# Performance work log

Hardware: AMD Instinct MI355X
Metric: run time of the kernel (lower is better)

Reference implementation:

```python
import jax, jax.numpy as jnp
import numpy as np

D_MODEL = 1024
NUM_HEADS = 16
HEAD_DIM = D_MODEL // NUM_HEADS
B, S = 4, 2048


def setup_inputs() -> dict:
    key = jax.random.key(0)
    ks = jax.random.split(key, 11)
    scale = 1.0 / np.sqrt(D_MODEL)
    inp = {
        "Q": jax.random.normal(ks[0], (B, S, D_MODEL), jnp.float32),
        "K": jax.random.normal(ks[1], (B, S, D_MODEL), jnp.float32),
        "V": jax.random.normal(ks[2], (B, S, D_MODEL), jnp.float32),
        # torch nn.Linear params: weight [out, in], bias [out]
        "WQ_w": jax.random.uniform(ks[3], (D_MODEL, D_MODEL), jnp.float32, -scale, scale),
        "WQ_b": jax.random.uniform(ks[4], (D_MODEL,), jnp.float32, -scale, scale),
        "WK_w": jax.random.uniform(ks[5], (D_MODEL, D_MODEL), jnp.float32, -scale, scale),
        "WK_b": jax.random.uniform(ks[6], (D_MODEL,), jnp.float32, -scale, scale),
        "WV_w": jax.random.uniform(ks[7], (D_MODEL, D_MODEL), jnp.float32, -scale, scale),
        "WV_b": jax.random.uniform(ks[8], (D_MODEL,), jnp.float32, -scale, scale),
        "WO_w": jax.random.uniform(ks[9], (D_MODEL, D_MODEL), jnp.float32, -scale, scale),
        "WO_b": jax.random.uniform(ks[10], (D_MODEL,), jnp.float32, -scale, scale),
    }
    return inp


def _linear(x, w, b):
    # torch Linear: y = x @ w.T + b
    return jnp.einsum("bsd,ed->bse", x, w) + b


def _split_heads(x):
    b, s, _ = x.shape
    return x.reshape(b, s, NUM_HEADS, HEAD_DIM).transpose(0, 2, 1, 3)  # [B,H,S,hd]


def reference(Q, K, V, WQ_w, WQ_b, WK_w, WK_b, WV_w, WV_b, WO_w, WO_b):
    q = _split_heads(_linear(Q, WQ_w, WQ_b))  # [B,H,S,hd]
    k = _split_heads(_linear(K, WK_w, WK_b))
    v = _split_heads(_linear(V, WV_w, WV_b))
    scale = 1.0 / jnp.sqrt(jnp.asarray(HEAD_DIM, jnp.float32))
    scores = jnp.einsum("bhqd,bhkd->bhqk", q, k) * scale  # [B,H,S,S]
    attn = jax.nn.softmax(scores, axis=-1)
    ctx = jnp.einsum("bhqk,bhkd->bhqd", attn, v)  # [B,H,S,hd]
    ctx = ctx.transpose(0, 2, 1, 3).reshape(Q.shape[0], Q.shape[1], D_MODEL)
    out = _linear(ctx, WO_w, WO_b)
    return out, attn
```

## Files before the change

kernel.cpp:

```cpp
#include <hip/hip_runtime.h>
#include <hip/hip_fp16.h>

typedef _Float16 half_t;
typedef __attribute__((ext_vector_type(8))) _Float16 half8;
typedef __attribute__((ext_vector_type(4))) _Float16 half4;
typedef __attribute__((ext_vector_type(4))) float f32x4;

#define D_MODEL 1024
#define NHEAD 16
#define HDIM 64
#define BATCH 4
#define SEQ 2048
#define M_TOTAL (BATCH*SEQ)

#define BM 128
#define BN 128
#define BKK 32
#define LDT 40

template<int OUTMODE, bool A_HALF>
__global__ __launch_bounds__(256)
void gemm_bt(const void* __restrict__ Ap, const float* __restrict__ Bp,
             const float* __restrict__ bias, void* __restrict__ outp)
{
    __shared__ half_t As[BM * LDT];
    __shared__ half_t Bs[BN * LDT];

    const int lin = blockIdx.x;
    const int swz = (lin & 7) * 64 + (lin >> 3);
    const int bm  = (swz >> 3) * BM;
    const int bn  = (swz & 7) * BN;

    const int tid  = threadIdx.x;
    const int lane = tid & 63;
    const int w    = tid >> 6;
    const int wm   = w >> 1, wn = w & 1;
    const int g    = lane >> 4, c = lane & 15;
    const int K    = 1024;

    f32x4 acc[4][4] = {};

    float4 fa[4];
    float4 fb[4];
    uint4  ha[2];

    auto load_tile = [&](int kt) {
        const int kb = kt * BKK;
        if (A_HALF) {
            const half_t* A = (const half_t*)Ap;
#pragma unroll
            for (int i = 0; i < 2; ++i) {
                const int row = (tid >> 2) + i * 64;
                const int col = (tid & 3) * 8;
                ha[i] = *(const uint4*)&A[(size_t)(bm + row) * K + kb + col];
            }
        } else {
            const float* A = (const float*)Ap;
#pragma unroll
            for (int i = 0; i < 4; ++i) {
                const int row = (tid >> 3) + i * 32;
                const int col = (tid & 7) * 4;
                fa[i] = *(const float4*)&A[(size_t)(bm + row) * K + kb + col];
            }
        }
#pragma unroll
        for (int i = 0; i < 4; ++i) {
            const int row = (tid >> 3) + i * 32;
            const int col = (tid & 7) * 4;
            fb[i] = *(const float4*)&Bp[(size_t)(bn + row) * K + kb + col];
        }
    };

    auto store_tile = [&]() {
        if (A_HALF) {
#pragma unroll
            for (int i = 0; i < 2; ++i) {
                const int row = (tid >> 2) + i * 64;
                const int col = (tid & 3) * 8;
                *(uint4*)&As[row * LDT + col] = ha[i];
            }
        } else {
#pragma unroll
            for (int i = 0; i < 4; ++i) {
                const int row = (tid >> 3) + i * 32;
                const int col = (tid & 7) * 4;
                half4 h = { (half_t)fa[i].x, (half_t)fa[i].y, (half_t)fa[i].z, (half_t)fa[i].w };
                *(half4*)&As[row * LDT + col] = h;
            }
        }
#pragma unroll
        for (int i = 0; i < 4; ++i) {
            const int row = (tid >> 3) + i * 32;
            const int col = (tid & 7) * 4;
            half4 h = { (half_t)fb[i].x, (half_t)fb[i].y, (half_t)fb[i].z, (half_t)fb[i].w };
            *(half4*)&Bs[row * LDT + col] = h;
        }
    };

    load_tile(0);
    const int NT = K / BKK;
    for (int kt = 0; kt < NT; ++kt) {
        __syncthreads();
        store_tile();
        __syncthreads();
        if (kt + 1 < NT) load_tile(kt + 1);

        half8 af[4], bf[4];
#pragma unroll
        for (int mt = 0; mt < 4; ++mt)
            af[mt] = *(const half8*)&As[(wm * 64 + mt * 16 + c) * LDT + g * 8];
#pragma unroll
        for (int nt = 0; nt < 4; ++nt)
            bf[nt] = *(const half8*)&Bs[(wn * 64 + nt * 16 + c) * LDT + g * 8];
        __builtin_amdgcn_s_setprio(1);
#pragma unroll
        for (int mt = 0; mt < 4; ++mt)
#pragma unroll
            for (int nt = 0; nt < 4; ++nt)
                acc[mt][nt] = __builtin_amdgcn_mfma_f32_16x16x32_f16(af[mt], bf[nt], acc[mt][nt], 0, 0, 0);
        __builtin_amdgcn_s_setprio(0);
    }

#pragma unroll
    for (int mt = 0; mt < 4; ++mt)
#pragma unroll
        for (int nt = 0; nt < 4; ++nt)
#pragma unroll
            for (int j = 0; j < 4; ++j) {
                const int gm = bm + wm * 64 + mt * 16 + g * 4 + j;
                const int gn = bn + wn * 64 + nt * 16 + c;
                const float val = acc[mt][nt][j] + bias[gn];
                if (OUTMODE == 0) {
                    const int b = gm >> 11, s = gm & 2047, h = gn >> 6, d = gn & 63;
                    ((half_t*)outp)[((size_t)(b * NHEAD + h) * SEQ + s) * HDIM + d] = (half_t)val;
                } else if (OUTMODE == 1) {
                    const int b = gm >> 11, s = gm & 2047, h = gn >> 6, d = gn & 63;
                    ((half_t*)outp)[((size_t)(b * NHEAD + h) * HDIM + d) * SEQ + s] = (half_t)val;
                } else {
                    ((float*)outp)[(size_t)gm * 1024 + gn] = val;
                }
            }
}

__global__ __launch_bounds__(256)
void attn_stats(const half_t* __restrict__ qh, const half_t* __restrict__ kh,
                float* __restrict__ inv_l)
{
    const int bid0 = blockIdx.x;
    const int bid  = (bid0 & 7) * 64 + (bid0 >> 3);
    const int bh   = bid >> 3;
    const int qb   = bid & 7;
    const int tid  = threadIdx.x;
    const int w    = tid >> 6;
    const int lane = tid & 63;
    const int g    = lane >> 4, c = lane & 15;
    const int wbase = qb * 256 + w * 64;
    const size_t hoff = (size_t)bh * SEQ * HDIM;

    half8 a0[4], a1[4];
#pragma unroll
    for (int rt = 0; rt < 4; ++rt) {
        a0[rt] = *(const half8*)&qh[hoff + (size_t)(wbase + rt * 16 + c) * HDIM + g * 8];
        a1[rt] = *(const half8*)&qh[hoff + (size_t)(wbase + rt * 16 + c) * HDIM + g * 8 + 32];
    }

    float l[4][4] = {};
#pragma unroll 2
    for (int t = 0; t < 128; ++t) {
        const int kc = t * 16;
        const half8 b0 = *(const half8*)&kh[hoff + (size_t)(kc + c) * HDIM + g * 8];
        const half8 b1 = *(const half8*)&kh[hoff + (size_t)(kc + c) * HDIM + g * 8 + 32];
#pragma unroll
        for (int rt = 0; rt < 4; ++rt) {
            f32x4 acc = {};
            acc = __builtin_amdgcn_mfma_f32_16x16x32_f16(a0[rt], b0, acc, 0, 0, 0);
            acc = __builtin_amdgcn_mfma_f32_16x16x32_f16(a1[rt], b1, acc, 0, 0, 0);
#pragma unroll
            for (int j = 0; j < 4; ++j)
                l[rt][j] += __expf(acc[j] * 0.125f);
        }
    }

#pragma unroll
    for (int rt = 0; rt < 4; ++rt)
#pragma unroll
        for (int j = 0; j < 4; ++j) {
            float v = l[rt][j];
            v += __shfl_xor(v, 1);
            v += __shfl_xor(v, 2);
            v += __shfl_xor(v, 4);
            v += __shfl_xor(v, 8);
            l[rt][j] = v;
        }
    if (c == 0) {
#pragma unroll
        for (int rt = 0; rt < 4; ++rt)
#pragma unroll
            for (int j = 0; j < 4; ++j)
                inv_l[bh * SEQ + wbase + rt * 16 + g * 4 + j] = 1.0f / l[rt][j];
    }
}

#define KPAD 88
#define VPAD 40
#define PPADX 40

__global__ __launch_bounds__(256)
void attn_pv(const half_t* __restrict__ qh, const half_t* __restrict__ kh,
             const half_t* __restrict__ vT, const float* __restrict__ inv_l,
             float* __restrict__ attn, half_t* __restrict__ ctx)
{
    __shared__ half_t Ks[2][32][KPAD];
    __shared__ half_t Vs[2][64][VPAD];
    __shared__ half_t pbuf[4][2][16][PPADX];

    const int bid0 = blockIdx.x;
    const int bid  = (bid0 & 7) * 128 + (bid0 >> 3);
    const int bh   = bid >> 4;
    const int qb   = bid & 15;
    const int tid  = threadIdx.x;
    const int w    = tid >> 6;
    const int lane = tid & 63;
    const int g    = lane >> 4, c = lane & 15;
    const int qbase = qb * 128;
    const int wbase = qbase + w * 32;
    const size_t hoff = (size_t)bh * SEQ * HDIM;

    half8 a0[2], a1[2];
#pragma unroll
    for (int rt = 0; rt < 2; ++rt) {
        a0[rt] = *(const half8*)&qh[hoff + (size_t)(wbase + rt * 16 + c) * HDIM + g * 8];
        a1[rt] = *(const half8*)&qh[hoff + (size_t)(wbase + rt * 16 + c) * HDIM + g * 8 + 32];
    }
    float inv[2][4];
#pragma unroll
    for (int rt = 0; rt < 2; ++rt)
#pragma unroll
        for (int j = 0; j < 4; ++j)
            inv[rt][j] = inv_l[bh * SEQ + wbase + rt * 16 + g * 4 + j];

    const half_t* vbase = vT + (size_t)bh * HDIM * SEQ;
    float* arow = attn + ((size_t)bh * SEQ + qbase) * SEQ;

    const int krow = tid >> 3;
    const int kcol = (tid & 7) * 8;
    const int vrow = tid >> 2;
    const int vcol = (tid & 3) * 8;

    const int srow = lane >> 3;
    const int scol = (lane & 7) * 4;

    uint4 kreg = *(const uint4*)&kh[hoff + (size_t)krow * HDIM + kcol];
    uint4 vreg = *(const uint4*)&vbase[(size_t)vrow * SEQ + vcol];
    *(uint4*)&Ks[0][krow][kcol] = kreg;
    *(uint4*)&Vs[0][vrow][vcol] = vreg;
    __syncthreads();

    f32x4 cacc[2][4] = {};

    for (int ch = 0; ch < 64; ++ch) {
        const int buf = ch & 1;
        const int cbase = ch * 32;

        const int ncb = (cbase + 32) & (SEQ - 1);
        kreg = *(const uint4*)&kh[hoff + (size_t)(ncb + krow) * HDIM + kcol];
        vreg = *(const uint4*)&vbase[(size_t)vrow * SEQ + ncb + vcol];

#pragma unroll
        for (int rt = 0; rt < 2; ++rt)
#pragma unroll
            for (int ct = 0; ct < 2; ++ct) {
                const half8 b0 = *(const half8*)&Ks[buf][ct * 16 + c][g * 8];
                const half8 b1 = *(const half8*)&Ks[buf][ct * 16 + c][g * 8 + 32];
                f32x4 acc = {};
                acc = __builtin_amdgcn_mfma_f32_16x16x32_f16(a0[rt], b0, acc, 0, 0, 0);
                acc = __builtin_amdgcn_mfma_f32_16x16x32_f16(a1[rt], b1, acc, 0, 0, 0);
#pragma unroll
                for (int j = 0; j < 4; ++j) {
                    const float p = __expf(acc[j] * 0.125f) * inv[rt][j];
                    pbuf[w][rt][g * 4 + j][ct * 16 + c] = (half_t)p;
                }
            }

#pragma unroll
        for (int rt = 0; rt < 2; ++rt)
#pragma unroll
            for (int hh = 0; hh < 2; ++hh) {
                const int r = hh * 8 + srow;
                const half4 hv = *(const half4*)&pbuf[w][rt][r][scol];
                f32x4 fv = { (float)hv[0], (float)hv[1], (float)hv[2], (float)hv[3] };
                *(f32x4*)&arow[(size_t)(w * 32 + rt * 16 + r) * SEQ + cbase + scol] = fv;
            }

        {
            half8 vb[4];
#pragma unroll
            for (int nt = 0; nt < 4; ++nt)
                vb[nt] = *(const half8*)&Vs[buf][nt * 16 + c][g * 8];
#pragma unroll
            for (int rt = 0; rt < 2; ++rt) {
                const half8 pa = *(const half8*)&pbuf[w][rt][c][g * 8];
                __builtin_amdgcn_s_setprio(1);
#pragma unroll
                for (int nt = 0; nt < 4; ++nt)
                    cacc[rt][nt] = __builtin_amdgcn_mfma_f32_16x16x32_f16(pa, vb[nt], cacc[rt][nt], 0, 0, 0);
                __builtin_amdgcn_s_setprio(0);
            }
        }

        __syncthreads();
        *(uint4*)&Ks[buf ^ 1][krow][kcol] = kreg;
        *(uint4*)&Vs[buf ^ 1][vrow][vcol] = vreg;
        __syncthreads();
    }

    const int b = bh >> 4, h = bh & 15;
#pragma unroll
    for (int rt = 0; rt < 2; ++rt)
#pragma unroll
        for (int nt = 0; nt < 4; ++nt)
#pragma unroll
            for (int j = 0; j < 4; ++j)
                ctx[(size_t)(b * SEQ + qbase + w * 32 + rt * 16 + g * 4 + j) * D_MODEL
                    + h * HDIM + nt * 16 + c] = (half_t)cacc[rt][nt][j];
}

extern "C" void kernel_launch(void* const* d_in, const int* in_sizes, int n_in,
                              void* d_out, int out_size, void* d_ws, size_t ws_size,
                              hipStream_t stream) {
    const float* Qin = (const float*)d_in[0];
    const float* Kin = (const float*)d_in[1];
    const float* Vin = (const float*)d_in[2];
    const float* WQw = (const float*)d_in[3];
    const float* WQb = (const float*)d_in[4];
    const float* WKw = (const float*)d_in[5];
    const float* WKb = (const float*)d_in[6];
    const float* WVw = (const float*)d_in[7];
    const float* WVb = (const float*)d_in[8];
    const float* WOw = (const float*)d_in[9];
    const float* WOb = (const float*)d_in[10];

    char* ws = (char*)d_ws;
    const size_t MB = 1024 * 1024;
    half_t* qh  = (half_t*)(ws);
    half_t* kh  = (half_t*)(ws + 16 * MB);
    half_t* vT  = (half_t*)(ws + 32 * MB);
    half_t* ctx = (half_t*)(ws + 48 * MB);

    float* out   = (float*)d_out;
    float* attn  = out + (size_t)M_TOTAL * D_MODEL;
    float* inv_l = out;

    dim3 blk(256);
    hipLaunchKernelGGL((gemm_bt<0, false>), dim3(512), blk, 0, stream, Qin, WQw, WQb, qh);
    hipLaunchKernelGGL((gemm_bt<0, false>), dim3(512), blk, 0, stream, Kin, WKw, WKb, kh);
    hipLaunchKernelGGL((gemm_bt<1, false>), dim3(512), blk, 0, stream, Vin, WVw, WVb, vT);
    hipLaunchKernelGGL(attn_stats, dim3(512), blk, 0, stream, qh, kh, inv_l);
    hipLaunchKernelGGL(attn_pv, dim3(1024), blk, 0, stream, qh, kh, vT, inv_l, attn, ctx);
    hipLaunchKernelGGL((gemm_bt<2, true>), dim3(512), blk, 0, stream, ctx, WOw, WOb, out);
}
```

Before: 513.9 us.

## Batch attn probability writes over 128-column spans and single-buffer K/V tiles

The attention-PV kernel now buffers probabilities for four 32-key chunks in a wider per-wave LDS buffer and writes the fp32 attn matrix once per 128 columns, in place of once per 32-column chunk. K/V shared tiles drop from double to single buffering, which keeps LDS usage in check despite the larger probability buffer. The goal is to separate the large attn global stores from the MFMA/exp inner loop and make them longer per row. Single buffering still relies on two barriers per chunk, and the stores now arrive in bursts.

Measured after the change: 544.8 us. +6.0%, slower.

```diff
diff --git a/kernel.cpp b/kernel.cpp
--- a/kernel.cpp
+++ b/kernel.cpp
@@ -203,16 +203,16 @@
 
 #define KPAD 88
 #define VPAD 40
-#define PPADX 40
+#define PBW  136
 
 __global__ __launch_bounds__(256)
 void attn_pv(const half_t* __restrict__ qh, const half_t* __restrict__ kh,
              const half_t* __restrict__ vT, const float* __restrict__ inv_l,
              float* __restrict__ attn, half_t* __restrict__ ctx)
 {
-    __shared__ half_t Ks[2][32][KPAD];
-    __shared__ half_t Vs[2][64][VPAD];
-    __shared__ half_t pbuf[4][2][16][PPADX];
+    __shared__ half_t Ks[32][KPAD];
+    __shared__ half_t Vs[64][VPAD];
+    __shared__ half_t pbuf[4][2][16][PBW];
 
     const int bid0 = blockIdx.x;
     const int bid  = (bid0 & 7) * 128 + (bid0 >> 3);
@@ -252,66 +252,74 @@
 
     uint4 kreg = *(const uint4*)&kh[hoff + (size_t)krow * HDIM + kcol];
     uint4 vreg = *(const uint4*)&vbase[(size_t)vrow * SEQ + vcol];
-    *(uint4*)&Ks[0][krow][kcol] = kreg;
-    *(uint4*)&Vs[0][vrow][vcol] = vreg;
+    *(uint4*)&Ks[krow][kcol] = kreg;
+    *(uint4*)&Vs[vrow][vcol] = vreg;
     __syncthreads();
 
     f32x4 cacc[2][4] = {};
 
-    for (int ch = 0; ch < 64; ++ch) {
-        const int buf = ch & 1;
-        const int cbase = ch * 32;
-
-        const int ncb = (cbase + 32) & (SEQ - 1);
-        kreg = *(const uint4*)&kh[hoff + (size_t)(ncb + krow) * HDIM + kcol];
-        vreg = *(const uint4*)&vbase[(size_t)vrow * SEQ + ncb + vcol];
-
-#pragma unroll
-        for (int rt = 0; rt < 2; ++rt)
-#pragma unroll
-            for (int ct = 0; ct < 2; ++ct) {
-                const half8 b0 = *(const half8*)&Ks[buf][ct * 16 + c][g * 8];
-                const half8 b1 = *(const half8*)&Ks[buf][ct * 16 + c][g * 8 + 32];
-                f32x4 acc = {};
-                acc = __builtin_amdgcn_mfma_f32_16x16x32_f16(a0[rt], b0, acc, 0, 0, 0);
-                acc = __builtin_amdgcn_mfma_f32_16x16x32_f16(a1[rt], b1, acc, 0, 0, 0);
-#pragma unroll
-                for (int j = 0; j < 4; ++j) {
-                    const float p = __expf(acc[j] * 0.125f) * inv[rt][j];
-                    pbuf[w][rt][g * 4 + j][ct * 16 + c] = (half_t)p;
+#pragma unroll 1
+    for (int sc = 0; sc < 16; ++sc) {
+#pragma unroll
+        for (int sub = 0; sub < 4; ++sub) {
+            const int cbase = sc * 128 + sub * 32;
+            const int ncb = (cbase + 32) & (SEQ - 1);
+
+            kreg = *(const uint4*)&kh[hoff + (size_t)(ncb + krow) * HDIM + kcol];
+            vreg = *(const uint4*)&vbase[(size_t)vrow * SEQ + ncb + vcol];
+
+#pragma unroll
+            for (int rt = 0; rt < 2; ++rt)
+#pragma unroll
+                for (int ct = 0; ct < 2; ++ct) {
+                    const half8 b0 = *(const half8*)&Ks[ct * 16 + c][g * 8];
+                    const half8 b1 = *(const half8*)&Ks[ct * 16 + c][g * 8 + 32];
+                    f32x4 acc = {};
+                    acc = __builtin_amdgcn_mfma_f32_16x16x32_f16(a0[rt], b0, acc, 0, 0, 0);
+                    acc = __builtin_amdgcn_mfma_f32_16x16x32_f16(a1[rt], b1, acc, 0, 0, 0);
+#pragma unroll
+                    for (int j = 0; j < 4; ++j) {
+                        const float p = __expf(acc[j] * 0.125f) * inv[rt][j];
+                        pbuf[w][rt][g * 4 + j][sub * 32 + ct * 16 + c] = (half_t)p;
+                    }
                 }
-            }
-
+
+            {
+                half8 vb[4];
+#pragma unroll
+                for (int nt = 0; nt < 4; ++nt)
+                    vb[nt] = *(const half8*)&Vs[nt * 16 + c][g * 8];
+#pragma unroll
+                for (int rt = 0; rt < 2; ++rt) {
+                    const half8 pa = *(const half8*)&pbuf[w][rt][c][sub * 32 + g * 8];
+                    __builtin_amdgcn_s_setprio(1);
+#pragma unroll
+                    for (int nt = 0; nt < 4; ++nt)
+                        cacc[rt][nt] = __builtin_amdgcn_mfma_f32_16x16x32_f16(pa, vb[nt], cacc[rt][nt], 0, 0, 0);
+                    __builtin_amdgcn_s_setprio(0);
+                }
+            }
+
+            __syncthreads();
+            *(uint4*)&Ks[krow][kcol] = kreg;
+            *(uint4*)&Vs[vrow][vcol] = vreg;
+            __syncthreads();
+        }
+
+        const int colb = sc * 128;
 #pragma unroll
         for (int rt = 0; rt < 2; ++rt)
 #pragma unroll
             for (int hh = 0; hh < 2; ++hh) {
                 const int r = hh * 8 + srow;
-                const half4 hv = *(const half4*)&pbuf[w][rt][r][scol];
-                f32x4 fv = { (float)hv[0], (float)hv[1], (float)hv[2], (float)hv[3] };
-                *(f32x4*)&arow[(size_t)(w * 32 + rt * 16 + r) * SEQ + cbase + scol] = fv;
-            }
-
-        {
-            half8 vb[4];
-#pragma unroll
-            for (int nt = 0; nt < 4; ++nt)
-                vb[nt] = *(const half8*)&Vs[buf][nt * 16 + c][g * 8];
-#pragma unroll
-            for (int rt = 0; rt < 2; ++rt) {
-                const half8 pa = *(const half8*)&pbuf[w][rt][c][g * 8];
-                __builtin_amdgcn_s_setprio(1);
-#pragma unroll
-                for (int nt = 0; nt < 4; ++nt)
-                    cacc[rt][nt] = __builtin_amdgcn_mfma_f32_16x16x32_f16(pa, vb[nt], cacc[rt][nt], 0, 0, 0);
-                __builtin_amdgcn_s_setprio(0);
-            }
-        }
-
-        __syncthreads();
-        *(uint4*)&Ks[buf ^ 1][krow][kcol] = kreg;
-        *(uint4*)&Vs[buf ^ 1][vrow][vcol] = vreg;
-        __syncthreads();
+                float* rowp = &arow[(size_t)(w * 32 + rt * 16 + r) * SEQ + colb];
+#pragma unroll
+                for (int cc = 0; cc < 4; ++cc) {
+                    const half4 hv = *(const half4*)&pbuf[w][rt][r][cc * 32 + scol];
+                    f32x4 fv = { (float)hv[0], (float)hv[1], (float)hv[2], (float)hv[3] };
+                    *(f32x4*)&rowp[cc * 32 + scol] = fv;
+                }
+            }
     }
 
     const int b = bh >> 4, h = bh & 15;
```
